# Kernel tuning notes

Hardware: AMD Instinct MI355X
Metric: run time of the kernel (lower is better)

The kernel has to match this reference:

```python
import jax, jax.numpy as jnp
import numpy as np

B, C, H, W = 2, 512, 64, 64
NUM_GROUPS = 32
EPS = 1e-6


def setup_inputs() -> dict:
    key = jax.random.key(0)
    ks = jax.random.split(key, 6)
    s = 1.0 / np.sqrt(C)
    return {
        "x": jax.random.normal(ks[0], (B, C, H, W), dtype=jnp.float32),
        "gn_scale": jnp.ones((C,), jnp.float32),
        "gn_bias": jnp.zeros((C,), jnp.float32),
        "wq": jax.random.normal(ks[1], (C, C), jnp.float32) * s,
        "bq": jnp.zeros((C,), jnp.float32),
        "wk": jax.random.normal(ks[2], (C, C), jnp.float32) * s,
        "bk": jnp.zeros((C,), jnp.float32),
        "wv": jax.random.normal(ks[3], (C, C), jnp.float32) * s,
        "bv": jnp.zeros((C,), jnp.float32),
        "wp": jax.random.normal(ks[4], (C, C), jnp.float32) * s,
        "bp": jnp.zeros((C,), jnp.float32),
    }


def group_norm(x, scale, bias):
    # x: [b, c, h, w]; GroupNorm with NUM_GROUPS groups, eps=1e-6, affine
    b, c, h, w = x.shape
    xg = x.reshape(b, NUM_GROUPS, c // NUM_GROUPS, h, w)
    mean = jnp.mean(xg, axis=(2, 3, 4), keepdims=True)
    var = jnp.var(xg, axis=(2, 3, 4), keepdims=True)
    xg = (xg - mean) * jax.lax.rsqrt(var + EPS)
    xn = xg.reshape(b, c, h, w)
    return xn * scale[None, :, None, None] + bias[None, :, None, None]


def reference(x, gn_scale, gn_bias, wq, bq, wk, bk, wv, bv, wp, bp):
    b, c, h, w = x.shape
    n = h * w
    hn = group_norm(x, gn_scale, gn_bias).reshape(b, c, n)  # [b,c,n]
    # 1x1 convs == per-pixel linear over channels
    q = jnp.einsum('dc,bcn->bdn', wq, hn) + bq[None, :, None]
    k = jnp.einsum('dc,bcn->bdn', wk, hn) + bk[None, :, None]
    v = jnp.einsum('dc,bcn->bdn', wv, hn) + bv[None, :, None]
    # attn[b,i,j] = softmax_j( q[:, :, i] . k[:, :, j] / sqrt(c) )
    attn = jnp.einsum('bci,bcj->bij', q, k) * (float(c) ** -0.5)
    attn = jax.nn.softmax(attn, axis=-1)
    out = jnp.einsum('bcj,bij->bci', v, attn)  # [b,c,n]
    out = jnp.einsum('dc,bcn->bdn', wp, out) + bp[None, :, None]
    return x + out.reshape(b, c, h, w)
```

## Files before the change

### kernel.cpp

```cpp
#include <hip/hip_runtime.h>

typedef __bf16 bf16x8 __attribute__((ext_vector_type(8)));
typedef float f32x4 __attribute__((ext_vector_type(4)));
typedef int i32x8 __attribute__((ext_vector_type(8)));


#if defined(__has_builtin)
#if __has_builtin(__builtin_amdgcn_global_load_lds)
#define HAS_GLL 1
#endif
#endif

__device__ __forceinline__ void async_copy16(const void* g, void* l) {
#ifdef HAS_GLL
    __builtin_amdgcn_global_load_lds(
        (const __attribute__((address_space(1))) unsigned int*)g,
        (__attribute__((address_space(3))) unsigned int*)l, 16, 0, 0);
#else
    *(int4*)l = *(const int4*)g;
#endif
}

__device__ __forceinline__ unsigned char to_fp8(float v) {
    return (unsigned char)(__builtin_amdgcn_cvt_pk_fp8_f32(v, v, 0, false) & 0xFF);
}

#define MXSCALE 0x7F7F7F7F

#define ASM_VMCNT(N) asm volatile("s_waitcnt vmcnt(" #N ")" ::: "memory")
#define ASM_LGKM0() asm volatile("s_waitcnt lgkmcnt(0)" ::: "memory")

__global__ __launch_bounds__(256) void prep_kernel(
    const float* __restrict__ x, float* __restrict__ ps,
    const float* __restrict__ wq, const float* __restrict__ wk,
    const float* __restrict__ wv, const float* __restrict__ wp,
    const float* __restrict__ bq, const float* __restrict__ bk,
    unsigned char* __restrict__ wqk8, unsigned char* __restrict__ wv8,
    __bf16* __restrict__ wp_b, float* __restrict__ bqk) {
    if (blockIdx.x >= 1024) {
        int idx = (blockIdx.x - 1024) * 256 + threadIdx.x;
        wqk8[idx] = to_fp8(wq[idx]);
        wqk8[262144 + idx] = to_fp8(wk[idx]);
        wv8[idx] = to_fp8(wv[idx]);
        wp_b[idx] = (__bf16)wp[idx];
        if (idx < 512) {
            bqk[idx] = bq[idx];
            bqk[512 + idx] = bk[idx];
        }
        return;
    }
    int blk = blockIdx.x;
    const float4* base = (const float4*)x + (size_t)blk * 1024;
    float s1 = 0.f, s2 = 0.f;
#pragma unroll
    for (int i = 0; i < 4; ++i) {
        float4 v = base[threadIdx.x + (i << 8)];
        s1 += v.x + v.y + v.z + v.w;
        s2 += v.x * v.x + v.y * v.y + v.z * v.z + v.w * v.w;
    }
    for (int off = 32; off >= 1; off >>= 1) {
        s1 += __shfl_xor(s1, off);
        s2 += __shfl_xor(s2, off);
    }
    __shared__ float r1[4], r2[4];
    int wave = threadIdx.x >> 6, lane = threadIdx.x & 63;
    if (lane == 0) { r1[wave] = s1; r2[wave] = s2; }
    __syncthreads();
    if (threadIdx.x == 0) {
        ps[blk] = r1[0] + r1[1] + r1[2] + r1[3];
        ps[1024 + blk] = r2[0] + r2[1] + r2[2] + r2[3];
    }
}

__global__ __launch_bounds__(256) void gn_apply_kernel(const float* __restrict__ x,
                                                       const float* __restrict__ gn_scale,
                                                       const float* __restrict__ gn_bias,
                                                       const float* __restrict__ ps,
                                                       unsigned char* __restrict__ hn8) {
    __shared__ float tile[32][33];
    int b = blockIdx.z;
    int n0 = blockIdx.x * 32, c0 = blockIdx.y * 32;
    int tx = threadIdx.x & 31, ty = threadIdx.x >> 5;
    const float* xb = x + (size_t)b * 512 * 4096;
#pragma unroll
    for (int r = 0; r < 4; ++r) {
        int c = ty + r * 8;
        tile[c][tx] = xb[(size_t)(c0 + c) * 4096 + n0 + tx];
    }
    int c = c0 + tx;
    int g = (b << 5) + (c >> 4);
    float s1 = 0.f, s2 = 0.f;
#pragma unroll
    for (int i = 0; i < 16; ++i) {
        s1 += ps[(g << 4) + i];
        s2 += ps[1024 + (g << 4) + i];
    }
    float m = s1 * (1.f / 65536.f);
    float var = s2 * (1.f / 65536.f) - m * m;
    float rs = rsqrtf(var + 1e-6f);
    float sc = gn_scale[c] * rs;
    float bi = gn_bias[c] - m * sc;
    __syncthreads();
    unsigned char* outp = hn8 + (size_t)b * 4096 * 512;
#pragma unroll
    for (int r = 0; r < 4; ++r) {
        int n = ty + r * 8;
        float v = tile[tx][n];
        outp[(size_t)(n0 + n) * 512 + c] = to_fp8(v * sc + bi);
    }
}

template <int BN, int OUT_MODE, int BIAS_MODE>
__device__ __forceinline__ void mx_gemm_body(
    const unsigned char* __restrict__ Ab, int lda,
    const unsigned char* __restrict__ Bb, int ldb,
    void* __restrict__ C, int ldc,
    const float* __restrict__ bias, int K, float scale,
    long m0, long n0, unsigned char* As, unsigned char* Bs) {
    constexpr int NT = BN / 32;
    constexpr int BSZ = BN * 128;
    const int tid = threadIdx.x;
    const int lane = tid & 63, wave = tid >> 6;
    const int ln = lane & 15, q = lane >> 4;
    const int wm = (wave >> 1) << 6;
    const int wn = (wave & 1) * (BN / 2);

    f32x4 acc[4][NT] = {};

    auto stage = [&](int kt, int buf) {
        const int k0 = kt << 7;
        unsigned char* Ad = As + buf * 16384;
        unsigned char* Bd = Bs + buf * BSZ;
#pragma unroll
        for (int p = 0; p < 4; ++p) {
            int c = (p << 8) + tid;
            int row = c >> 3, sg = ((c & 7) ^ (row & 7)) << 4;
            async_copy16(Ab + (long)row * lda + k0 + sg, Ad + (c << 4));
        }
#pragma unroll
        for (int p = 0; p < NT; ++p) {
            int c = (p << 8) + tid;
            int row = c >> 3, sg = ((c & 7) ^ (row & 7)) << 4;
            async_copy16(Bb + (long)row * ldb + k0 + sg, Bd + (c << 4));
        }
    };

    const int nk = K >> 7;
    stage(0, 0);
    if (nk > 1) stage(1, 1);

    for (int ki = 0; ki < nk; ++ki) {
        if (ki < nk - 1) {
            if constexpr (NT == 4) ASM_VMCNT(8);
            else ASM_VMCNT(6);
        } else {
            ASM_VMCNT(0);
        }
        __builtin_amdgcn_s_barrier();
        const int cur = ki & 1;
        const unsigned char* Ar = As + cur * 16384;
        const unsigned char* Br = Bs + cur * BSZ;
        i32x8 af[4], bf[NT];
#pragma unroll
        for (int t = 0; t < 4; ++t) {
            int row = wm + t * 16 + ln, e = row & 7;
            const unsigned char* ap = Ar + (row << 7);
            *(int4*)&af[t] = *(const int4*)(ap + ((((q << 1)) ^ e) << 4));
            *((int4*)&af[t] + 1) = *(const int4*)(ap + ((((q << 1) | 1) ^ e) << 4));
        }
#pragma unroll
        for (int t = 0; t < NT; ++t) {
            int row = wn + t * 16 + ln, e = row & 7;
            const unsigned char* bp = Br + (row << 7);
            *(int4*)&bf[t] = *(const int4*)(bp + ((((q << 1)) ^ e) << 4));
            *((int4*)&bf[t] + 1) = *(const int4*)(bp + ((((q << 1) | 1) ^ e) << 4));
        }
        ASM_LGKM0();
        __builtin_amdgcn_s_barrier();
        if (ki + 2 < nk) stage(ki + 2, cur);
        __builtin_amdgcn_s_setprio(1);
#pragma unroll
        for (int mt = 0; mt < 4; ++mt)
#pragma unroll
            for (int nt = 0; nt < NT; ++nt)
                acc[mt][nt] = __builtin_amdgcn_mfma_scale_f32_16x16x128_f8f6f4(
                    af[mt], bf[nt], acc[mt][nt], 0, 0, 0, MXSCALE, 0, MXSCALE);
        __builtin_amdgcn_s_setprio(0);
    }

#pragma unroll
    for (int mt = 0; mt < 4; ++mt) {
#pragma unroll
        for (int nt = 0; nt < NT; ++nt) {
            long col = n0 + wn + nt * 16 + ln;
#pragma unroll
            for (int r = 0; r < 4; ++r) {
                long row = m0 + wm + mt * 16 + (q << 2) + r;
                float v = acc[mt][nt][r] * scale;
                if (BIAS_MODE == 1) v += bias[row];
                if (BIAS_MODE == 2) v += bias[col];
                long off = row * (long)ldc + col;
                if (OUT_MODE == 0) {
                    ((unsigned char*)C)[off] = to_fp8(v);
                } else if (OUT_MODE == 1) {
                    ((_Float16*)C)[off] = (_Float16)v;
                } else {
                    ((__bf16*)C)[off] = (__bf16)v;
                }
            }
        }
    }
}

__global__ __launch_bounds__(256) void qkv_kernel(
    const unsigned char* __restrict__ hn8, const unsigned char* __restrict__ wqk8,
    const unsigned char* __restrict__ wv8, const float* __restrict__ bqk,
    const float* __restrict__ bv, unsigned char* __restrict__ qk8,
    unsigned char* __restrict__ v8) {
    __shared__ __align__(16) unsigned char As[2 * 128 * 128];
    __shared__ __align__(16) unsigned char Bs[2 * 128 * 128];
    int z = blockIdx.z;
    if (z < 2) {
        long b = z;
        long m0 = (long)blockIdx.y * 128, n0 = (long)blockIdx.x * 128;
        mx_gemm_body<128, 0, 2>(hn8 + b * 4096 * 512 + m0 * 512, 512,
                                wqk8 + n0 * 512, 512,
                                qk8 + b * 4096 * 1024, 1024,
                                bqk, 512, 1.f, m0, n0, As, Bs);
    } else {
        long b = z - 2;
        int flat = blockIdx.y * 8 + blockIdx.x;
        long m0 = (long)(flat >> 6) * 128, n0 = (long)(flat & 63) * 64;
        mx_gemm_body<64, 0, 1>(wv8 + m0 * 512, 512,
                               hn8 + b * 4096 * 512 + n0 * 512, 512,
                               v8 + b * 512 * 4096, 4096,
                               bv, 512, 1.f, m0, n0, As, Bs);
    }
}

__global__ __launch_bounds__(256) void mx_s_softmax_kernel(
    const unsigned char* __restrict__ QK, unsigned char* __restrict__ P8,
    float* __restrict__ pmaxF, float* __restrict__ psumF, float scale) {
    __shared__ __align__(16) unsigned char As[2 * 128 * 128];
    __shared__ __align__(16) unsigned char Bs[2 * 128 * 128];
    __shared__ float sm_max[2][128], sm_sum[2][128];
    int id = (blockIdx.x & 7) * 256 + (blockIdx.x >> 3);
    int mg = id >> 5;
    long b = mg >> 5;
    int panel = mg & 31;
    long j0 = (long)panel * 128;
    long i0 = (long)(id & 31) * 128;
    const unsigned char* Ab = QK + b * 4096 * 1024 + j0 * 1024 + 512;
    const unsigned char* Bb = QK + b * 4096 * 1024 + i0 * 1024;

    const int tid = threadIdx.x;
    const int lane = tid & 63, wave = tid >> 6;
    const int ln = lane & 15, q = lane >> 4;
    const int wm = (wave >> 1) << 6;
    const int wn = (wave & 1) * 64;

    f32x4 acc[4][4] = {};

    auto stage = [&](int kt, int buf) {
        const int k0 = kt << 7;
        unsigned char* Ad = As + buf * 16384;
        unsigned char* Bd = Bs + buf * 16384;
#pragma unroll
        for (int p = 0; p < 4; ++p) {
            int c = (p << 8) + tid;
            int row = c >> 3, sg = ((c & 7) ^ (row & 7)) << 4;
            async_copy16(Ab + (long)row * 1024 + k0 + sg, Ad + (c << 4));
        }
#pragma unroll
        for (int p = 0; p < 4; ++p) {
            int c = (p << 8) + tid;
            int row = c >> 3, sg = ((c & 7) ^ (row & 7)) << 4;
            async_copy16(Bb + (long)row * 1024 + k0 + sg, Bd + (c << 4));
        }
    };

    stage(0, 0);
    stage(1, 1);
    for (int ki = 0; ki < 4; ++ki) {
        if (ki < 3) ASM_VMCNT(8);
        else ASM_VMCNT(0);
        __builtin_amdgcn_s_barrier();
        const int cur = ki & 1;
        const unsigned char* Ar = As + cur * 16384;
        const unsigned char* Br = Bs + cur * 16384;
        i32x8 af[4], bf[4];
#pragma unroll
        for (int t = 0; t < 4; ++t) {
            int row = wm + t * 16 + ln, e = row & 7;
            const unsigned char* ap = Ar + (row << 7);
            *(int4*)&af[t] = *(const int4*)(ap + ((((q << 1)) ^ e) << 4));
            *((int4*)&af[t] + 1) = *(const int4*)(ap + ((((q << 1) | 1) ^ e) << 4));
        }
#pragma unroll
        for (int t = 0; t < 4; ++t) {
            int row = wn + t * 16 + ln, e = row & 7;
            const unsigned char* bp = Br + (row << 7);
            *(int4*)&bf[t] = *(const int4*)(bp + ((((q << 1)) ^ e) << 4));
            *((int4*)&bf[t] + 1) = *(const int4*)(bp + ((((q << 1) | 1) ^ e) << 4));
        }
        ASM_LGKM0();
        __builtin_amdgcn_s_barrier();
        if (ki + 2 < 4) stage(ki + 2, cur);
        __builtin_amdgcn_s_setprio(1);
#pragma unroll
        for (int mt = 0; mt < 4; ++mt)
#pragma unroll
            for (int nt = 0; nt < 4; ++nt)
                acc[mt][nt] = __builtin_amdgcn_mfma_scale_f32_16x16x128_f8f6f4(
                    af[mt], bf[nt], acc[mt][nt], 0, 0, 0, MXSCALE, 0, MXSCALE);
        __builtin_amdgcn_s_setprio(0);
    }

    const float C_ = scale * 1.4426950408889634f;
#pragma unroll
    for (int mt = 0; mt < 4; ++mt)
#pragma unroll
        for (int nt = 0; nt < 4; ++nt)
#pragma unroll
            for (int r = 0; r < 4; ++r) acc[mt][nt][r] *= C_;

#pragma unroll
    for (int nt = 0; nt < 4; ++nt) {
        float m = acc[0][nt][0];
#pragma unroll
        for (int mt = 0; mt < 4; ++mt)
#pragma unroll
            for (int r = 0; r < 4; ++r) m = fmaxf(m, acc[mt][nt][r]);
        m = fmaxf(m, __shfl_xor(m, 16));
        m = fmaxf(m, __shfl_xor(m, 32));
        if (lane < 16) sm_max[wave >> 1][wn + nt * 16 + ln] = m;
    }
    __syncthreads();

    unsigned int* rp = (unsigned int*)As;
    float mtl[4];
#pragma unroll
    for (int nt = 0; nt < 4; ++nt) {
        const int i = wn + nt * 16 + ln;
        mtl[nt] = ceilf(fmaxf(sm_max[0][i], sm_max[1][i]));
        float s = 0.f;
#pragma unroll
        for (int mt = 0; mt < 4; ++mt) {
            float p0 = exp2f(acc[mt][nt][0] - mtl[nt]);
            float p1 = exp2f(acc[mt][nt][1] - mtl[nt]);
            float p2 = exp2f(acc[mt][nt][2] - mtl[nt]);
            float p3 = exp2f(acc[mt][nt][3] - mtl[nt]);
            s += (p0 + p1) + (p2 + p3);
            int w = __builtin_amdgcn_cvt_pk_fp8_f32(p0, p1, 0, false);
            w = __builtin_amdgcn_cvt_pk_fp8_f32(p2, p3, w, true);
            int jq = ((wave >> 1) << 4) + (mt << 2) + q;
            rp[i * 32 + (jq ^ ((i & 7) << 2))] = (unsigned int)w;
        }
        s += __shfl_xor(s, 16);
        s += __shfl_xor(s, 32);
        if (lane < 16) sm_sum[wave >> 1][i] = s;
    }
    __syncthreads();

    if (wave < 2 && lane < 16) {
#pragma unroll
        for (int nt = 0; nt < 4; ++nt) {
            int i = wn + nt * 16 + ln;
            long rowg = b * 4096 + i0 + i;
            pmaxF[rowg * 32 + panel] = mtl[nt];
            psumF[rowg * 32 + panel] = sm_sum[0][i] + sm_sum[1][i];
        }
    }

    {
        const int i = tid >> 1, half = tid & 1;
        const unsigned int* rr = rp + i * 32;
        unsigned char* Pw = P8 + b * 4096 * 4096 + (i0 + i) * 4096 + j0 + half * 64;
#pragma unroll
        for (int k = 0; k < 4; ++k) {
            int js = (half * 16 + 4 * k) ^ ((i & 7) << 2);
            *(int4*)(Pw + k * 16) = *(const int4*)(rr + js);
        }
    }
}

__global__ __launch_bounds__(256) void mx_pv_scaled_kernel(
    const unsigned char* __restrict__ P, const unsigned char* __restrict__ V,
    const float* __restrict__ pmaxF, const float* __restrict__ psumF,
    __bf16* __restrict__ O) {
    __shared__ __align__(16) unsigned char As[2 * 128 * 128];
    __shared__ __align__(16) unsigned char Bs[2 * 64 * 128];
    __shared__ __align__(16) unsigned char sb_lds[128 * 32];
    __shared__ float inv_lds[128];
    const int tid = threadIdx.x;
    const int lane = tid & 63, wave = tid >> 6;
    const int ln = lane & 15, q = lane >> 4;
    const int wm = (wave >> 1) << 6, wn = (wave & 1) << 5;
    const int b = blockIdx.x >> 5;
    const long m0 = (long)(blockIdx.x & 31) * 128;
    const long n0 = (long)blockIdx.y * 64;
    const long rowg0 = (long)b * 4096 + m0;

    if (tid < 128) {
        const float4* pm4 = (const float4*)(pmaxF + (rowg0 + tid) * 32);
        const float4* ps4 = (const float4*)(psumF + (rowg0 + tid) * 32);
        float4 pm[8], ps[8];
#pragma unroll
        for (int i = 0; i < 8; ++i) { pm[i] = pm4[i]; ps[i] = ps4[i]; }
        float g = -1e30f;
#pragma unroll
        for (int i = 0; i < 8; ++i)
            g = fmaxf(g, fmaxf(fmaxf(pm[i].x, pm[i].y), fmaxf(pm[i].z, pm[i].w)));
        float denom = 0.f;
        unsigned int* sbw = (unsigned int*)sb_lds + tid * 8;
#pragma unroll
        for (int i = 0; i < 8; ++i) {
            float d0 = pm[i].x - g, d1 = pm[i].y - g, d2 = pm[i].z - g, d3 = pm[i].w - g;
            denom += ps[i].x * exp2f(d0) + ps[i].y * exp2f(d1) +
                     ps[i].z * exp2f(d2) + ps[i].w * exp2f(d3);
            int b0 = 127 + (int)d0, b1 = 127 + (int)d1, b2 = 127 + (int)d2, b3 = 127 + (int)d3;
            b0 = b0 < 0 ? 0 : b0; b1 = b1 < 0 ? 0 : b1;
            b2 = b2 < 0 ? 0 : b2; b3 = b3 < 0 ? 0 : b3;
            sbw[i] = (unsigned)b0 | ((unsigned)b1 << 8) | ((unsigned)b2 << 16) |
                     ((unsigned)b3 << 24);
        }
        inv_lds[tid] = 1.f / denom;
    }
    __syncthreads();

    const unsigned char* Pb = P + rowg0 * 4096;
    const unsigned char* Vb = V + ((long)b * 512 + n0) * 4096;

    f32x4 acc[4][2] = {};

    auto stage = [&](int kt, int buf) {
        const int k0 = kt << 7;
        unsigned char* Ad = As + buf * 16384;
        unsigned char* Bd = Bs + buf * 8192;
#pragma unroll
        for (int p = 0; p < 4; ++p) {
            int c = (p << 8) + tid;
            int row = c >> 3, sg = ((c & 7) ^ (row & 7)) << 4;
            async_copy16(Pb + (long)row * 4096 + k0 + sg, Ad + (c << 4));
        }
#pragma unroll
        for (int p = 0; p < 2; ++p) {
            int c = (p << 8) + tid;
            int row = c >> 3, sg = ((c & 7) ^ (row & 7)) << 4;
            async_copy16(Vb + (long)row * 4096 + k0 + sg, Bd + (c << 4));
        }
    };

    stage(0, 0);
    stage(1, 1);
    for (int ki = 0; ki < 32; ++ki) {
        if (ki < 31) ASM_VMCNT(6);
        else ASM_VMCNT(0);
        __builtin_amdgcn_s_barrier();
        const int cur = ki & 1;
        const unsigned char* Ar = As + cur * 16384;
        const unsigned char* Br = Bs + cur * 8192;
        i32x8 af[4], bf[2];
        int saw[4];
#pragma unroll
        for (int t = 0; t < 4; ++t) {
            int row = wm + t * 16 + ln, e = row & 7;
            const unsigned char* ap = Ar + (row << 7);
            *(int4*)&af[t] = *(const int4*)(ap + ((((q << 1)) ^ e) << 4));
            *((int4*)&af[t] + 1) = *(const int4*)(ap + ((((q << 1) | 1) ^ e) << 4));
            saw[t] = (int)sb_lds[(row << 5) + ki] * 0x01010101;
        }
#pragma unroll
        for (int t = 0; t < 2; ++t) {
            int row = wn + t * 16 + ln, e = row & 7;
            const unsigned char* bp = Br + (row << 7);
            *(int4*)&bf[t] = *(const int4*)(bp + ((((q << 1)) ^ e) << 4));
            *((int4*)&bf[t] + 1) = *(const int4*)(bp + ((((q << 1) | 1) ^ e) << 4));
        }
        ASM_LGKM0();
        __builtin_amdgcn_s_barrier();
        if (ki + 2 < 32) stage(ki + 2, cur);
        __builtin_amdgcn_s_setprio(1);
#pragma unroll
        for (int mt = 0; mt < 4; ++mt)
#pragma unroll
            for (int nt = 0; nt < 2; ++nt)
                acc[mt][nt] = __builtin_amdgcn_mfma_scale_f32_16x16x128_f8f6f4(
                    af[mt], bf[nt], acc[mt][nt], 0, 0, 0, saw[mt], 0, MXSCALE);
        __builtin_amdgcn_s_setprio(0);
    }

    __bf16* Ob = O + (long)b * 4096 * 512;
#pragma unroll
    for (int mt = 0; mt < 4; ++mt) {
#pragma unroll
        for (int nt = 0; nt < 2; ++nt) {
            long col = n0 + wn + nt * 16 + ln;
#pragma unroll
            for (int r = 0; r < 4; ++r) {
                int rowl = wm + mt * 16 + (q << 2) + r;
                Ob[(m0 + rowl) * 512 + col] = (__bf16)(acc[mt][nt][r] * inv_lds[rowl]);
            }
        }
    }
}

__global__ __launch_bounds__(256) void proj_kernel(
    const __bf16* __restrict__ A, const __bf16* __restrict__ Bt, long bsB,
    float* __restrict__ C, long bsC, const float* __restrict__ bias,
    const float* __restrict__ resid) {
    __shared__ __align__(16) __bf16 As[128][64];
    __shared__ __align__(16) __bf16 Bs[64][64];
    const int tid = threadIdx.x;
    const int wave = tid >> 6, lane = tid & 63;
    const int q = lane >> 4, ln = lane & 15;
    const int wm = wave << 5;
    const long m0 = (long)blockIdx.y * 128, n0 = (long)blockIdx.x * 64;
    const int b = blockIdx.z;
    const __bf16* Ab = A + m0 * 512;
    const __bf16* Bb = Bt + (long)b * bsB + n0 * 512;

    f32x4 acc[2][4] = {};

    for (int k0 = 0; k0 < 512; k0 += 64) {
        __syncthreads();
#pragma unroll
        for (int p = 0; p < 4; ++p) {
            int c = (p << 8) + tid;
            int row = c >> 3, sg = (c & 7) << 3;
            async_copy16(Ab + (long)row * 512 + k0 + sg, &As[0][0] + (c << 3));
        }
#pragma unroll
        for (int p = 0; p < 2; ++p) {
            int c = (p << 8) + tid;
            int row = c >> 3, sg = (c & 7) << 3;
            async_copy16(Bb + (long)row * 512 + k0 + sg, &Bs[0][0] + (c << 3));
        }
        __syncthreads();
#pragma unroll
        for (int kk = 0; kk < 2; ++kk) {
            bf16x8 af[2], bfr[4];
#pragma unroll
            for (int mt = 0; mt < 2; ++mt)
                af[mt] = *(const bf16x8*)(&As[wm + mt * 16 + ln][(kk << 5) + (q << 3)]);
#pragma unroll
            for (int nt = 0; nt < 4; ++nt)
                bfr[nt] = *(const bf16x8*)(&Bs[nt * 16 + ln][(kk << 5) + (q << 3)]);
#pragma unroll
            for (int mt = 0; mt < 2; ++mt)
#pragma unroll
                for (int nt = 0; nt < 4; ++nt)
                    acc[mt][nt] = __builtin_amdgcn_mfma_f32_16x16x32_bf16(
                        af[mt], bfr[nt], acc[mt][nt], 0, 0, 0);
        }
    }

#pragma unroll
    for (int mt = 0; mt < 2; ++mt) {
#pragma unroll
        for (int nt = 0; nt < 4; ++nt) {
            long col = n0 + nt * 16 + ln;
#pragma unroll
            for (int r = 0; r < 4; ++r) {
                long row = m0 + wm + mt * 16 + (q << 2) + r;
                long off = (long)b * bsC + row * 4096 + col;
                C[off] = acc[mt][nt][r] + bias[row] + resid[off];
            }
        }
    }
}

extern "C" void kernel_launch(void* const* d_in, const int* in_sizes, int n_in,
                              void* d_out, int out_size, void* d_ws, size_t ws_size,
                              hipStream_t stream) {
    const float* x = (const float*)d_in[0];
    const float* gn_scale = (const float*)d_in[1];
    const float* gn_bias = (const float*)d_in[2];
    const float* wq = (const float*)d_in[3];
    const float* bq = (const float*)d_in[4];
    const float* wk = (const float*)d_in[5];
    const float* bk = (const float*)d_in[6];
    const float* wv = (const float*)d_in[7];
    const float* bv = (const float*)d_in[8];
    const float* wp = (const float*)d_in[9];
    const float* bp = (const float*)d_in[10];
    float* out = (float*)d_out;

    char* ws = (char*)d_ws;
    unsigned char* wqk8 = (unsigned char*)(ws + 0x0);
    unsigned char* wv8 = (unsigned char*)(ws + 0x80000);
    __bf16* wp_b = (__bf16*)(ws + 0xC0000);
    float* bqk = (float*)(ws + 0x140000);
    float* psum = (float*)(ws + 0x142000);
    unsigned char* hn8 = (unsigned char*)(ws + 0x150000);
    unsigned char* qk8 = (unsigned char*)(ws + 0x550000);
    unsigned char* v8 = (unsigned char*)(ws + 0xD50000);
    __bf16* o_t = (__bf16*)(ws + 0x1150000);
    unsigned char* S8 = (unsigned char*)(ws + 0x1950000);
    float* pmaxF = (float*)(ws + 0x3950000);
    float* psumF = (float*)(ws + 0x3A50000);
    (void)ws_size;

    prep_kernel<<<2048, 256, 0, stream>>>(x, psum, wq, wk, wv, wp, bq, bk,
                                          wqk8, wv8, wp_b, bqk);
    gn_apply_kernel<<<dim3(128, 16, 2), 256, 0, stream>>>(x, gn_scale, gn_bias,
                                                          psum, hn8);
    qkv_kernel<<<dim3(8, 32, 4), 256, 0, stream>>>(hn8, wqk8, wv8, bqk, bv,
                                                   qk8, v8);

    const float attn_scale = 0.044194173824159216f;
    mx_s_softmax_kernel<<<2048, 256, 0, stream>>>(qk8, S8, pmaxF, psumF,
                                                  attn_scale);
    mx_pv_scaled_kernel<<<dim3(64, 8), 256, 0, stream>>>(S8, v8, pmaxF, psumF,
                                                         o_t);

    proj_kernel<<<dim3(64, 4, 2), 256, 0, stream>>>(
        wp_b, o_t, 4096l * 512, out, 512l * 4096, bp, x);
}
```

Measured before the change: 195.6 us.

## Replace double-buffered async GEMM staging with single-buffer synchronous loop

Removes the two-stage LDS double buffering, with its manual vmcnt waits and prefetch of tile k+2, from the shared fp8 GEMM body and the QK softmax kernel. Each iteration now loads a single tile into one buffer between two __syncthreads calls. This halves LDS per block, which may allow more resident blocks per CU, but it gives up the overlap between global loads and MFMA compute.

```diff
diff --git a/kernel.cpp b/kernel.cpp
--- a/kernel.cpp
+++ b/kernel.cpp
@@ -118,7 +118,6 @@
     const float* __restrict__ bias, int K, float scale,
     long m0, long n0, unsigned char* As, unsigned char* Bs) {
     constexpr int NT = BN / 32;
-    constexpr int BSZ = BN * 128;
     const int tid = threadIdx.x;
     const int lane = tid & 63, wave = tid >> 6;
     const int ln = lane & 15, q = lane >> 4;
@@ -127,57 +126,38 @@
 
     f32x4 acc[4][NT] = {};
 
-    auto stage = [&](int kt, int buf) {
-        const int k0 = kt << 7;
-        unsigned char* Ad = As + buf * 16384;
-        unsigned char* Bd = Bs + buf * BSZ;
+    const int nk = K >> 7;
+    for (int ki = 0; ki < nk; ++ki) {
+        const int k0 = ki << 7;
+        __syncthreads();
 #pragma unroll
         for (int p = 0; p < 4; ++p) {
             int c = (p << 8) + tid;
             int row = c >> 3, sg = ((c & 7) ^ (row & 7)) << 4;
-            async_copy16(Ab + (long)row * lda + k0 + sg, Ad + (c << 4));
+            async_copy16(Ab + (long)row * lda + k0 + sg, &As[c << 4]);
         }
 #pragma unroll
         for (int p = 0; p < NT; ++p) {
             int c = (p << 8) + tid;
             int row = c >> 3, sg = ((c & 7) ^ (row & 7)) << 4;
-            async_copy16(Bb + (long)row * ldb + k0 + sg, Bd + (c << 4));
-        }
-    };
-
-    const int nk = K >> 7;
-    stage(0, 0);
-    if (nk > 1) stage(1, 1);
-
-    for (int ki = 0; ki < nk; ++ki) {
-        if (ki < nk - 1) {
-            if constexpr (NT == 4) ASM_VMCNT(8);
-            else ASM_VMCNT(6);
-        } else {
-            ASM_VMCNT(0);
-        }
-        __builtin_amdgcn_s_barrier();
-        const int cur = ki & 1;
-        const unsigned char* Ar = As + cur * 16384;
-        const unsigned char* Br = Bs + cur * BSZ;
+            async_copy16(Bb + (long)row * ldb + k0 + sg, &Bs[c << 4]);
+        }
+        __syncthreads();
         i32x8 af[4], bf[NT];
 #pragma unroll
         for (int t = 0; t < 4; ++t) {
             int row = wm + t * 16 + ln, e = row & 7;
-            const unsigned char* ap = Ar + (row << 7);
+            const unsigned char* ap = &As[row << 7];
             *(int4*)&af[t] = *(const int4*)(ap + ((((q << 1)) ^ e) << 4));
             *((int4*)&af[t] + 1) = *(const int4*)(ap + ((((q << 1) | 1) ^ e) << 4));
         }
 #pragma unroll
         for (int t = 0; t < NT; ++t) {
             int row = wn + t * 16 + ln, e = row & 7;
-            const unsigned char* bp = Br + (row << 7);
+            const unsigned char* bp = &Bs[row << 7];
             *(int4*)&bf[t] = *(const int4*)(bp + ((((q << 1)) ^ e) << 4));
             *((int4*)&bf[t] + 1) = *(const int4*)(bp + ((((q << 1) | 1) ^ e) << 4));
         }
-        ASM_LGKM0();
-        __builtin_amdgcn_s_barrier();
-        if (ki + 2 < nk) stage(ki + 2, cur);
         __builtin_amdgcn_s_setprio(1);
 #pragma unroll
         for (int mt = 0; mt < 4; ++mt)
@@ -217,8 +197,8 @@
     const unsigned char* __restrict__ wv8, const float* __restrict__ bqk,
     const float* __restrict__ bv, unsigned char* __restrict__ qk8,
     unsigned char* __restrict__ v8) {
-    __shared__ __align__(16) unsigned char As[2 * 128 * 128];
-    __shared__ __align__(16) unsigned char Bs[2 * 128 * 128];
+    __shared__ __align__(16) unsigned char As[128 * 128];
+    __shared__ __align__(16) unsigned char Bs[128 * 128];
     int z = blockIdx.z;
     if (z < 2) {
         long b = z;
@@ -241,8 +221,8 @@
 __global__ __launch_bounds__(256) void mx_s_softmax_kernel(
     const unsigned char* __restrict__ QK, unsigned char* __restrict__ P8,
     float* __restrict__ pmaxF, float* __restrict__ psumF, float scale) {
-    __shared__ __align__(16) unsigned char As[2 * 128 * 128];
-    __shared__ __align__(16) unsigned char Bs[2 * 128 * 128];
+    __shared__ __align__(16) unsigned char As[128 * 128];
+    __shared__ __align__(16) unsigned char Bs[128 * 128];
     __shared__ float sm_max[2][128], sm_sum[2][128];
     int id = (blockIdx.x & 7) * 256 + (blockIdx.x >> 3);
     int mg = id >> 5;
@@ -261,51 +241,37 @@
 
     f32x4 acc[4][4] = {};
 
-    auto stage = [&](int kt, int buf) {
-        const int k0 = kt << 7;
-        unsigned char* Ad = As + buf * 16384;
-        unsigned char* Bd = Bs + buf * 16384;
+    for (int ki = 0; ki < 4; ++ki) {
+        const int k0 = ki << 7;
+        __syncthreads();
 #pragma unroll
         for (int p = 0; p < 4; ++p) {
             int c = (p << 8) + tid;
             int row = c >> 3, sg = ((c & 7) ^ (row & 7)) << 4;
-            async_copy16(Ab + (long)row * 1024 + k0 + sg, Ad + (c << 4));
+            async_copy16(Ab + (long)row * 1024 + k0 + sg, &As[c << 4]);
         }
 #pragma unroll
         for (int p = 0; p < 4; ++p) {
             int c = (p << 8) + tid;
             int row = c >> 3, sg = ((c & 7) ^ (row & 7)) << 4;
-            async_copy16(Bb + (long)row * 1024 + k0 + sg, Bd + (c << 4));
-        }
-    };
-
-    stage(0, 0);
-    stage(1, 1);
-    for (int ki = 0; ki < 4; ++ki) {
-        if (ki < 3) ASM_VMCNT(8);
-        else ASM_VMCNT(0);
-        __builtin_amdgcn_s_barrier();
-        const int cur = ki & 1;
-        const unsigned char* Ar = As + cur * 16384;
-        const unsigned char* Br = Bs + cur * 16384;
+            async_copy16(Bb + (long)row * 1024 + k0 + sg, &Bs[c << 4]);
+        }
+        __syncthreads();
         i32x8 af[4], bf[4];
 #pragma unroll
         for (int t = 0; t < 4; ++t) {
             int row = wm + t * 16 + ln, e = row & 7;
-            const unsigned char* ap = Ar + (row << 7);
+            const unsigned char* ap = &As[row << 7];
             *(int4*)&af[t] = *(const int4*)(ap + ((((q << 1)) ^ e) << 4));
             *((int4*)&af[t] + 1) = *(const int4*)(ap + ((((q << 1) | 1) ^ e) << 4));
         }
 #pragma unroll
         for (int t = 0; t < 4; ++t) {
             int row = wn + t * 16 + ln, e = row & 7;
-            const unsigned char* bp = Br + (row << 7);
+            const unsigned char* bp = &Bs[row << 7];
             *(int4*)&bf[t] = *(const int4*)(bp + ((((q << 1)) ^ e) << 4));
             *((int4*)&bf[t] + 1) = *(const int4*)(bp + ((((q << 1) | 1) ^ e) << 4));
         }
-        ASM_LGKM0();
-        __builtin_amdgcn_s_barrier();
-        if (ki + 2 < 4) stage(ki + 2, cur);
         __builtin_amdgcn_s_setprio(1);
 #pragma unroll
         for (int mt = 0; mt < 4; ++mt)
```

Measured after the change: 187.1 us. 1.05x faster.
